# Performance work log

Measured on AMD Instinct MI355X. Metric: run time of the kernel, lower is better.

The kernel has to match this reference:

```python
import jax, jax.numpy as jnp
import numpy as np

B, L, H, V = 256, 4096, 64, 64
LN_EPS = 1e-5


def setup_inputs() -> dict:
    key = jax.random.key(0)
    ks = jax.random.split(key, 12)
    s = 1.0 / np.sqrt(H)
    return {
        "seq": jax.random.randint(ks[0], (B, L), 0, V),
        "embed_W": jax.random.normal(ks[1], (V, H), jnp.float32),
        "ff_w1": jax.random.normal(ks[2], (H, 2 * H), jnp.float32) * s,
        "ff_b1": jnp.zeros((2 * H,), jnp.float32),
        "ff_w2": jax.random.normal(ks[3], (2 * H, H), jnp.float32) * s,
        "ff_b2": jnp.zeros((H,), jnp.float32),
        "ln_w": jnp.ones((H,), jnp.float32),
        "ln_b": jnp.zeros((H,), jnp.float32),
        "read_w": jax.random.normal(ks[4], (H, H), jnp.float32) * s,
        "read_b": jnp.zeros((H,), jnp.float32),
        "out_w": jax.random.normal(ks[5], (H, V), jnp.float32) * s,
        "out_b": jnp.zeros((V,), jnp.float32),
    }


def _layer_norm(x, w, b):
    mu = jnp.mean(x, axis=-1, keepdims=True)
    var = jnp.mean(jnp.square(x - mu), axis=-1, keepdims=True)
    return (x - mu) * jax.lax.rsqrt(var + LN_EPS) * w + b


def reference(seq, embed_W, ff_w1, ff_b1, ff_w2, ff_b2, ln_w, ln_b,
              read_w, read_b, out_w, out_b):
    h = embed_W[seq]  # (B, L, H)
    ff = jax.nn.relu(h @ ff_w1 + ff_b1) @ ff_w2 + ff_b2
    h = _layer_norm(h + ff, ln_w, ln_b)

    def step(M, k):  # M: (B,H,H), k: (B,H)
        v_pred = jnp.einsum('bij,bj->bi', M, k)
        denom = jnp.sum(k * k, axis=-1, keepdims=True) + 1e-6
        dv = k - v_pred / denom
        M = M + dv[:, :, None] * k[:, None, :]  # rank-1 delta write
        return M, None

    ks = jnp.swapaxes(h[:, :-1, :], 0, 1)  # (L-1, B, H)
    M0 = jnp.zeros((h.shape[0], h.shape[-1], h.shape[-1]), h.dtype)
    M, _ = jax.lax.scan(step, M0, ks)

    q = h[:, -1, :]
    ctx = jnp.einsum('bij,bj->bi', M, q)
    return (ctx @ read_w + read_b) @ out_w + out_b  # (B, V)
```

## Files before the change

kernel.cpp:

```cpp
#include <hip/hip_runtime.h>
#include <hip/hip_bf16.h>

#define LN_EPS 1e-5f

static __device__ __forceinline__ float readlane_f(float v, int lane) {
    return __int_as_float(__builtin_amdgcn_readlane(__float_as_int(v), lane));
}
static __device__ __forceinline__ void writelane_f(int& dst, float val, int lane_imm) {
    asm("v_writelane_b32 %0, %1, %2"
        : "+v"(dst)
        : "s"(__float_as_int(val)), "i"(lane_imm));
}

__global__ __launch_bounds__(64) void build_keys(
    const float* __restrict__ embed,
    const float* __restrict__ w1,
    const float* __restrict__ b1,
    const float* __restrict__ w2,
    const float* __restrict__ b2,
    const float* __restrict__ lnw,
    const float* __restrict__ lnb,
    float* __restrict__ keytab)
{
    const int v = blockIdx.x, lane = threadIdx.x;
    __shared__ float se[64];
    __shared__ float sh[128];
    se[lane] = embed[v * 64 + lane];
    __syncthreads();
    float h0 = b1[lane];
    float h1 = b1[lane + 64];
    #pragma unroll 8
    for (int i = 0; i < 64; ++i) {
        float e = se[i];
        h0 = fmaf(e, w1[i * 128 + lane], h0);
        h1 = fmaf(e, w1[i * 128 + lane + 64], h1);
    }
    sh[lane]      = fmaxf(h0, 0.f);
    sh[lane + 64] = fmaxf(h1, 0.f);
    __syncthreads();
    float acc = b2[lane];
    #pragma unroll 8
    for (int j = 0; j < 128; ++j)
        acc = fmaf(sh[j], w2[j * 64 + lane], acc);
    float pre = se[lane] + acc;
    float sum = pre;
    #pragma unroll
    for (int off = 32; off >= 1; off >>= 1) sum += __shfl_xor(sum, off, 64);
    float mu  = sum * (1.f / 64.f);
    float dev = pre - mu;
    float sq  = dev * dev;
    #pragma unroll
    for (int off = 32; off >= 1; off >>= 1) sq += __shfl_xor(sq, off, 64);
    float var = sq * (1.f / 64.f);
    float key = dev * (1.f / sqrtf(var + LN_EPS)) * lnw[lane] + lnb[lane];
    keytab[v * 64 + lane] = key;
}

__global__ __launch_bounds__(64) void build_tables(
    const float* __restrict__ keytab,
    const float* __restrict__ read_w,
    const float* __restrict__ read_b,
    const float* __restrict__ out_w,
    const float* __restrict__ out_b,
    float* __restrict__ Gg,
    float* __restrict__ GhatN,
    float* __restrict__ Wc,
    float* __restrict__ biasv)
{
    const int w = blockIdx.x, lane = threadIdx.x;
    __shared__ float sk[64 * 65];
    __shared__ float srw[64];
    #pragma unroll 8
    for (int r = 0; r < 64; ++r) sk[r * 65 + lane] = keytab[r * 64 + lane];
    srw[lane] = read_w[w * 64 + lane];
    __syncthreads();
    float g = 0.f;
    #pragma unroll 8
    for (int i = 0; i < 64; ++i)
        g = fmaf(sk[w * 65 + i], sk[lane * 65 + i], g);
    float gww  = readlane_f(g, w);
    float beta = 1.f / (gww + 1e-6f);
    Gg[w * 64 + lane]    = g;
    GhatN[w * 64 + lane] = -(beta * g);
    float acc = 0.f;
    #pragma unroll 8
    for (int j = 0; j < 64; ++j)
        acc = fmaf(srw[j], out_w[j * 64 + lane], acc);
    Wc[w * 64 + lane] = acc;
    if (w == 0) {
        float bacc = out_b[lane];
        #pragma unroll 8
        for (int j = 0; j < 64; ++j)
            bacc = fmaf(read_b[j], out_w[j * 64 + lane], bacc);
        biasv[lane] = bacc;
    }
}

__global__ __launch_bounds__(64) void delta_scan(
    const int*   __restrict__ seq,
    const float* __restrict__ Gg,
    const float* __restrict__ GhatN,
    const float* __restrict__ keytab,
    const float* __restrict__ Wc,
    const float* __restrict__ biasv,
    float* __restrict__ out)
{
    const int lane = threadIdx.x;
    const int b    = blockIdx.x;
    __shared__ float sG[64 * 64];
    __shared__ float sc[64];
    __shared__ float sCtx[64];
    #pragma unroll 8
    for (int r = 0; r < 64; ++r) sG[r * 64 + lane] = GhatN[r * 64 + lane];
    sc[lane] = 0.f;
    const int* seqb = seq + (size_t)b * 4096;
    float d = Gg[seqb[4095] * 64 + lane];
    __syncthreads();

    int vS = 0;
    int vcur = seqb[64 * 63 + lane];
    int   wq[21];
    float q_[21];
    #pragma unroll
    for (int s = 0; s < 21; ++s) {
        wq[s] = __builtin_amdgcn_readlane(vcur, 62 - s);
        q_[s] = sG[wq[s] * 64 + lane];
    }

    #pragma unroll 1
    for (int blk = 64; blk >= 0; --blk) {
        int vnext = (blk > 0) ? seqb[(blk - 1) * 63 + lane] : vcur;
        #pragma unroll
        for (int j = 62; j >= 0; --j) {
            const int slot = (62 - j) % 21;
            const int jl   = j - 21;
            int   w0  = wq[slot];
            float row = q_[slot];
            float p   = readlane_f(d, w0);
            int wn = (jl >= 0) ? __builtin_amdgcn_readlane(vcur, jl)
                               : __builtin_amdgcn_readlane(vnext, jl + 63);
            wq[slot] = wn;
            q_[slot] = sG[wn * 64 + lane];
            d = fmaf(p, row, d);
            writelane_f(vS, p, j);
        }
        atomicAdd(&sc[vcur & 63], __int_as_float(vS));
        vS = 0;
        vcur = vnext;
    }
    __syncthreads();

    float ctx = 0.f;
    #pragma unroll 8
    for (int v = 0; v < 64; ++v)
        ctx = fmaf(sc[v], keytab[v * 64 + lane], ctx);
    sCtx[lane] = ctx;
    __syncthreads();
    float o = biasv[lane];
    #pragma unroll 8
    for (int i = 0; i < 64; ++i)
        o = fmaf(sCtx[i], Wc[i * 64 + lane], o);
    out[(size_t)b * 64 + lane] = o;
}

extern "C" void kernel_launch(void* const* d_in, const int* in_sizes, int n_in,
                              void* d_out, int out_size, void* d_ws, size_t ws_size,
                              hipStream_t stream) {
    const int*   seq    = (const int*)d_in[0];
    const float* embed  = (const float*)d_in[1];
    const float* ff_w1  = (const float*)d_in[2];
    const float* ff_b1  = (const float*)d_in[3];
    const float* ff_w2  = (const float*)d_in[4];
    const float* ff_b2  = (const float*)d_in[5];
    const float* ln_w   = (const float*)d_in[6];
    const float* ln_b   = (const float*)d_in[7];
    const float* read_w = (const float*)d_in[8];
    const float* read_b = (const float*)d_in[9];
    const float* out_w  = (const float*)d_in[10];
    const float* out_b  = (const float*)d_in[11];
    float* out = (float*)d_out;

    float* wsf    = (float*)d_ws;
    float* keytab = wsf;
    float* Gg     = wsf + 4096;
    float* GhatN  = wsf + 8192;
    float* Wc     = wsf + 12288;
    float* biasv  = wsf + 16384;

    build_keys<<<64, 64, 0, stream>>>(embed, ff_w1, ff_b1, ff_w2, ff_b2, ln_w, ln_b, keytab);
    build_tables<<<64, 64, 0, stream>>>(keytab, read_w, read_b, out_w, out_b,
                                        Gg, GhatN, Wc, biasv);
    delta_scan<<<256, 64, 0, stream>>>(seq, Gg, GhatN, keytab, Wc, biasv, out);
}
```

Measured before the change: 168.5 us.

## Pair scan steps to halve serial readlane-fma dependency chain

Processes two delta-rule scan steps per iteration. Both readlanes of the state vector are issued up front, and the second step's coefficient is corrected via an extra readlane of the first row (p2 + p1*g). This shortens the critical latency chain of dependent readlane→fma ops in the sequential scan. The cost is an extra readlane, an fma and slightly more live registers per pair, plus a readfirstlane in the writelane helper.

```diff
diff --git a/kernel.cpp b/kernel.cpp
--- a/kernel.cpp
+++ b/kernel.cpp
@@ -7,9 +7,10 @@
     return __int_as_float(__builtin_amdgcn_readlane(__float_as_int(v), lane));
 }
 static __device__ __forceinline__ void writelane_f(int& dst, float val, int lane_imm) {
+    int sval = __builtin_amdgcn_readfirstlane(__float_as_int(val));
     asm("v_writelane_b32 %0, %1, %2"
         : "+v"(dst)
-        : "s"(__float_as_int(val)), "i"(lane_imm));
+        : "s"(sval), "i"(lane_imm));
 }
 
 __global__ __launch_bounds__(64) void build_keys(
@@ -131,18 +132,36 @@
     for (int blk = 64; blk >= 0; --blk) {
         int vnext = (blk > 0) ? seqb[(blk - 1) * 63 + lane] : vcur;
         #pragma unroll
-        for (int j = 62; j >= 0; --j) {
-            const int slot = (62 - j) % 21;
-            const int jl   = j - 21;
-            int   w0  = wq[slot];
-            float row = q_[slot];
-            float p   = readlane_f(d, w0);
-            int wn = (jl >= 0) ? __builtin_amdgcn_readlane(vcur, jl)
-                               : __builtin_amdgcn_readlane(vnext, jl + 63);
-            wq[slot] = wn;
-            q_[slot] = sG[wn * 64 + lane];
-            d = fmaf(p, row, d);
-            writelane_f(vS, p, j);
+        for (int j = 62; j >= 2; j -= 2) {
+            const int s0  = (62 - j) % 21;
+            const int s1  = (63 - j) % 21;
+            const int jl0 = j - 21, jl1 = j - 22;
+            int   w0 = wq[s0],  w1 = wq[s1];
+            float row0 = q_[s0], row1 = q_[s1];
+            float p1 = readlane_f(d, w0);
+            float p2 = readlane_f(d, w1);
+            float g  = readlane_f(row0, w1);
+            int wn0 = (jl0 >= 0) ? __builtin_amdgcn_readlane(vcur, jl0)
+                                 : __builtin_amdgcn_readlane(vnext, jl0 + 63);
+            int wn1 = (jl1 >= 0) ? __builtin_amdgcn_readlane(vcur, jl1)
+                                 : __builtin_amdgcn_readlane(vnext, jl1 + 63);
+            wq[s0] = wn0; q_[s0] = sG[wn0 * 64 + lane];
+            wq[s1] = wn1; q_[s1] = sG[wn1 * 64 + lane];
+            float s_1 = fmaf(p1, g, p2);
+            d = fmaf(p1, row0, d);
+            d = fmaf(s_1, row1, d);
+            writelane_f(vS, p1, j);
+            writelane_f(vS, s_1, j - 1);
+        }
+        {
+            const int s0 = 20;
+            int   w0 = wq[s0];
+            float row0 = q_[s0];
+            float p1 = readlane_f(d, w0);
+            int wn0 = __builtin_amdgcn_readlane(vnext, 42);
+            wq[s0] = wn0; q_[s0] = sG[wn0 * 64 + lane];
+            d = fmaf(p1, row0, d);
+            writelane_f(vS, p1, 0);
         }
         atomicAdd(&sc[vcur & 63], __int_as_float(vS));
         vS = 0;
```

New measurement: 176.2 us. 1.05x slower.
